# Optimization experiments

Measured on AMD Instinct MI355X. Metric: run time of the kernel, lower is better.

## Reference

```python
import jax, jax.numpy as jnp
import numpy as np

WS = 7        # window size (cubic)
SHIFT = 3     # shift size (cubic)
NH = 6        # num heads
EPS = 1e-5


def _layernorm(x, g, b):
    m = x.mean(-1, keepdims=True)
    v = ((x - m) ** 2).mean(-1, keepdims=True)
    return (x - m) / jnp.sqrt(v + EPS) * g + b


def _win_partition(x, ws):
    # (B,H,W,T,C) -> (B*nW, ws^3, C)
    B, H, W, T, C = x.shape
    x = x.reshape(B, H // ws, ws, W // ws, ws, T // ws, ws, C)
    return x.transpose(0, 1, 3, 5, 2, 4, 6, 7).reshape(-1, ws * ws * ws, C)


def _win_reverse(w, ws, B, H, W, T):
    # (B*nW, ws^3, C) -> (B,H,W,T,C)
    C = w.shape[-1]
    x = w.reshape(B, H // ws, W // ws, T // ws, ws, ws, ws, C)
    return x.transpose(0, 1, 4, 2, 5, 3, 6, 7).reshape(B, H, W, T, C)


def _rel_index(ws):
    # 3D relative position index, (N, N) int, N = ws^3 (torch.meshgrid default 'ij')
    coords = np.stack(np.meshgrid(np.arange(ws), np.arange(ws), np.arange(ws), indexing='ij'))
    cf = coords.reshape(3, -1)
    rel = (cf[:, :, None] - cf[:, None, :]).transpose(1, 2, 0)
    rel[:, :, 0] += ws - 1
    rel[:, :, 1] += ws - 1
    rel[:, :, 2] += ws - 1
    rel[:, :, 0] *= (2 * ws - 1) ** 2
    rel[:, :, 1] *= (2 * ws - 1)
    return rel.sum(-1)


def _compute_mask(Hp, Wp, Tp, ws, shift):
    img = np.zeros((1, Hp, Wp, Tp, 1), np.float32)
    cnt = 0
    sl = (slice(0, -ws), slice(-ws, -shift), slice(-shift, None))
    for h in sl:
        for w in sl:
            for t in sl:
                img[:, h, w, t, :] = cnt
                cnt += 1
    mw = np.asarray(_win_partition(jnp.asarray(img), ws)).reshape(-1, ws ** 3)  # (nW, N)
    am = mw[:, None, :] - mw[:, :, None]
    return jnp.asarray(np.where(am != 0, -100.0, 0.0).astype(np.float32))


def setup_inputs() -> dict:
    key = jax.random.key(0)
    ks = jax.random.split(key, 10)
    B, Hd, Wd, Td, C = 2, 28, 28, 28, 192
    L = Hd * Wd * Td
    Ch = int(C * 4.0)
    s = 0.02
    inp = {
        'x': jax.random.normal(ks[0], (B, L, C), jnp.float32),
        'mask': _compute_mask(Hd, Wd, Td, WS, SHIFT),
        'gamma1': jnp.ones((C,), jnp.float32),
        'beta1': jnp.zeros((C,), jnp.float32),
        'qkv_w': jax.random.normal(ks[1], (3 * C, C), jnp.float32) * s,
        'qkv_b': jnp.zeros((3 * C,), jnp.float32),
        'rpb_table': jax.random.normal(ks[2], ((2 * WS - 1) ** 3, NH), jnp.float32) * s,
        'proj_w': jax.random.normal(ks[3], (C, C), jnp.float32) * s,
        'proj_b': jnp.zeros((C,), jnp.float32),
        'gamma2': jnp.ones((C,), jnp.float32),
        'beta2': jnp.zeros((C,), jnp.float32),
        'fc1_w': jax.random.normal(ks[4], (Ch, C), jnp.float32) * s,
        'fc1_b': jnp.zeros((Ch,), jnp.float32),
        'fc2_w': jax.random.normal(ks[5], (C, Ch), jnp.float32) * s,
        'fc2_b': jnp.zeros((C,), jnp.float32),
        'H': Hd, 'W': Wd, 'T': Td,
    }
    return inp


def reference(x, mask, gamma1, beta1, qkv_w, qkv_b, rpb_table, proj_w, proj_b,
              gamma2, beta2, fc1_w, fc1_b, fc2_w, fc2_b, H, W, T):
    B, L, C = x.shape
    hd = C // NH
    scale = hd ** -0.5
    shortcut = x

    h1 = _layernorm(x, gamma1, beta1).reshape(B, H, W, T, C)
    # H,W,T are multiples of WS -> no padding; cyclic shift for SW-MSA
    shifted = jnp.roll(h1, (-SHIFT, -SHIFT, -SHIFT), axis=(1, 2, 3))
    xw = _win_partition(shifted, WS)            # (B*nW, N, C)
    Bn, N, _ = xw.shape

    qkv = (xw @ qkv_w.T + qkv_b).reshape(Bn, N, 3, NH, hd).transpose(2, 0, 3, 1, 4)
    q, k, v = qkv[0] * scale, qkv[1], qkv[2]     # (Bn, NH, N, hd)
    attn = jnp.einsum('bhnd,bhmd->bhnm', q, k)   # (Bn, NH, N, N)

    idx = _rel_index(WS)
    bias = rpb_table[idx.reshape(-1)].reshape(N, N, NH).transpose(2, 0, 1)
    attn = attn + bias[None]

    nW = mask.shape[0]
    attn = attn.reshape(Bn // nW, nW, NH, N, N) + mask[None, :, None]
    attn = jax.nn.softmax(attn.reshape(Bn, NH, N, N), axis=-1)

    out = jnp.einsum('bhnm,bhmd->bhnd', attn, v).transpose(0, 2, 1, 3).reshape(Bn, N, C)
    out = out @ proj_w.T + proj_b

    shifted = _win_reverse(out, WS, B, H, W, T)
    xr = jnp.roll(shifted, (SHIFT, SHIFT, SHIFT), axis=(1, 2, 3)).reshape(B, L, C)

    x = shortcut + xr
    h2 = _layernorm(x, gamma2, beta2)
    m = jax.nn.gelu(h2 @ fc1_w.T + fc1_b, approximate=False)
    return x + (m @ fc2_w.T + fc2_b)
```

## Files before the change

### kernel.cpp

```cpp
#include <hip/hip_runtime.h>
#include <hip/hip_bf16.h>

typedef unsigned short u16;
typedef unsigned int u32;
typedef __attribute__((ext_vector_type(8))) short s16x8;
typedef __attribute__((ext_vector_type(4))) float f32x4;

__device__ __forceinline__ float bf2f(u16 v) {
    union { u32 u; float f; } x; x.u = ((u32)v) << 16; return x.f;
}
__device__ __forceinline__ u16 f2bf(float f) {
    union { float f; u32 u; } x; x.f = f;
    u32 r = x.u + 0x7fffu + ((x.u >> 16) & 1u);
    return (u16)(r >> 16);
}
__device__ __forceinline__ u32 f2bf_pk(float a, float b) {
    return (u32)f2bf(a) | ((u32)f2bf(b) << 16);
}
__device__ __forceinline__ void gl2lds(const u16* g, u16* l) {
    __builtin_amdgcn_global_load_lds(
        (const __attribute__((address_space(1))) unsigned int*)g,
        (__attribute__((address_space(3))) unsigned int*)l, 16, 0, 0);
}

#define L_TOK 21952
#define C_DIM 192
#define LOG2E 1.4426950408889634f
#define Q2SCALE 0.2550565444463649f
#define BT_STR 352

__global__ __launch_bounds__(256) void cvt_k(const float* __restrict__ s0,
                                             const float* __restrict__ s1,
                                             const float* __restrict__ s2,
                                             const float* __restrict__ s3,
                                             u16* __restrict__ dst)
{
    int i = blockIdx.x * 256 + threadIdx.x;
    float v;
    if (i < 110592) v = s0[i];
    else if (i < 147456) v = s1[i - 110592];
    else if (i < 294912) v = s2[i - 147456];
    else v = s3[i - 294912];
    dst[i] = f2bf(v);
}

__global__ __launch_bounds__(256) void bias6_k(const float* __restrict__ rpb,
                                               u16* __restrict__ bias6T)
{
    const int n = blockIdx.x * 256 + threadIdx.x;
    if (n >= BT_STR) return;
    const int m = blockIdx.y, hh = blockIdx.z;
    u16 v = 0;
    if (n <= 342) {
        int hq = n / 49, r1 = n - hq * 49, wq = r1 / 7, tq = r1 - wq * 7;
        int hm = m / 49, r2 = m - hm * 49, wm = r2 / 7, tm = r2 - wm * 7;
        int idx = ((hq - hm + 6) * 13 + (wq - wm + 6)) * 13 + (tq - tm + 6);
        v = f2bf(rpb[idx * 6 + hh] * LOG2E);
    }
    bias6T[((size_t)hh * 343 + m) * BT_STR + n] = v;
}

template<int MODE>
__global__ __launch_bounds__(256) void ln_k(const float* __restrict__ in,
                                            const float* __restrict__ g,
                                            const float* __restrict__ b,
                                            u16* __restrict__ out)
{
    const int lane = threadIdx.x & 63, wv = threadIdx.x >> 6;
    const int tok = blockIdx.x * 4 + wv;
    size_t base = (size_t)tok * C_DIM;
    float x0 = in[base + lane];
    float x1 = in[base + 64 + lane];
    float x2 = in[base + 128 + lane];
    float s = x0 + x1 + x2;
    float sq = x0 * x0 + x1 * x1 + x2 * x2;
    #pragma unroll
    for (int off = 32; off > 0; off >>= 1) {
        s += __shfl_xor(s, off, 64);
        sq += __shfl_xor(sq, off, 64);
    }
    const float mean = s * (1.0f / 192.0f);
    float var = sq * (1.0f / 192.0f) - mean * mean;
    var = fmaxf(var, 0.0f);
    const float rstd = rsqrtf(var + 1e-5f);

    size_t obase;
    if (MODE == 0) {
        int bi = tok / L_TOK;
        int l = tok - bi * L_TOK;
        int h = l / 784;
        int rm = l - h * 784;
        int w = rm / 28;
        int t = rm - w * 28;
        int hs = h + 25; if (hs >= 28) hs -= 28;
        int ws = w + 25; if (ws >= 28) ws -= 28;
        int ts = t + 25; if (ts >= 28) ts -= 28;
        int win = ((bi * 4 + hs / 7) * 4 + ws / 7) * 4 + ts / 7;
        int n = (hs % 7) * 49 + (ws % 7) * 7 + (ts % 7);
        obase = ((size_t)win * 343 + n) * C_DIM;
    } else {
        obase = base;
    }
    #pragma unroll
    for (int i = 0; i < 3; i++) {
        int c = lane + i * 64;
        float xv = (i == 0) ? x0 : (i == 1) ? x1 : x2;
        float y = (xv - mean) * rstd * g[c] + b[c];
        out[obase + c] = f2bf(y);
    }
}

template<int K, int EPI>
__global__ __launch_bounds__(256) void gemm_k(const u16* __restrict__ A,
                                              const u16* __restrict__ W,
                                              const float* __restrict__ bias,
                                              void* __restrict__ outp,
                                              const void* __restrict__ resp,
                                              int Ncols)
{
    __shared__ __align__(16) u16 As[3 * 128 * 32];
    __shared__ __align__(16) u16 Bs[3 * 64 * 32];
    const int t = threadIdx.x;
    const int bm = blockIdx.y;
    const int n0 = blockIdx.x * 64;
    const int lane = t & 63, wv = t >> 6;
    const int wm = (wv >> 1) * 64, wn = (wv & 1) * 32;
    const int r16 = lane & 15, quad = lane >> 4;

    f32x4 acc[4][2];
    #pragma unroll
    for (int i = 0; i < 4; i++)
        #pragma unroll
        for (int j = 0; j < 2; j++) acc[i][j] = (f32x4){0.f, 0.f, 0.f, 0.f};

    const int ar = t >> 2, ac = (t & 3) * 8;
    const size_t abase = (size_t)bm * 128 * K;

    for (int kc = 0; kc < K; kc += 96) {
        if (kc) __syncthreads();
        #pragma unroll
        for (int kt = 0; kt < 3; kt++) {
            const int k0 = kc + kt * 32;
            gl2lds(&A[abase + (size_t)ar * K + k0 + ac], &As[kt * 4096 + 8 * t]);
            gl2lds(&A[abase + (size_t)(ar + 64) * K + k0 + ac], &As[kt * 4096 + 2048 + 8 * t]);
            gl2lds(&W[(size_t)(n0 + ar) * K + k0 + ac], &Bs[kt * 2048 + 8 * t]);
        }
        __syncthreads();
        #pragma unroll
        for (int kt = 0; kt < 3; kt++) {
            s16x8 af[4], bf[2];
            #pragma unroll
            for (int fm = 0; fm < 4; fm++)
                af[fm] = *(const s16x8*)&As[kt * 4096 + (wm + fm * 16 + r16) * 32 + quad * 8];
            #pragma unroll
            for (int fn = 0; fn < 2; fn++)
                bf[fn] = *(const s16x8*)&Bs[kt * 2048 + (wn + fn * 16 + r16) * 32 + quad * 8];
            #pragma unroll
            for (int fm = 0; fm < 4; fm++)
                #pragma unroll
                for (int fn = 0; fn < 2; fn++)
                    acc[fm][fn] = __builtin_amdgcn_mfma_f32_16x16x32_bf16(af[fm], bf[fn], acc[fm][fn], 0, 0, 0);
        }
    }

    #pragma unroll
    for (int fm = 0; fm < 4; fm++) {
        #pragma unroll
        for (int fn = 0; fn < 2; fn++) {
            #pragma unroll
            for (int r = 0; r < 4; r++) {
                const int grow = bm * 128 + wm + fm * 16 + quad * 4 + r;
                const int gcol = n0 + wn + fn * 16 + r16;
                float v = acc[fm][fn][r] + bias[gcol];
                if (EPI == 0) {
                    if (gcol < 192) v *= Q2SCALE;
                    ((u16*)outp)[(size_t)grow * Ncols + gcol] = f2bf(v);
                } else if (EPI == 1) {
                    v = 0.5f * v * (1.0f + erff(v * 0.70710678118654752f));
                    ((u16*)outp)[(size_t)grow * Ncols + gcol] = f2bf(v);
                } else if (EPI == 2) {
                    size_t o = (size_t)grow * C_DIM + gcol;
                    ((float*)outp)[o] = v + ((const float*)resp)[o];
                } else {
                    int win = grow / 343, n = grow - win * 343;
                    int bi = win >> 6, wi = win & 63;
                    int hw = wi >> 4, ww = (wi >> 2) & 3, tw = wi & 3;
                    int ph = n / 49, rem = n - ph * 49;
                    int pw = rem / 7, pt = rem - pw * 7;
                    int h = hw * 7 + ph + 3; if (h >= 28) h -= 28;
                    int w = ww * 7 + pw + 3; if (w >= 28) w -= 28;
                    int tt = tw * 7 + pt + 3; if (tt >= 28) tt -= 28;
                    int l = (h * 28 + w) * 28 + tt;
                    size_t o = ((size_t)bi * L_TOK + l) * C_DIM + gcol;
                    ((float*)outp)[o] = v + ((const float*)resp)[o];
                }
            }
        }
    }
}

__global__ __launch_bounds__(256, 2) void attn_k(const u16* __restrict__ qkv,
                                                 const u16* __restrict__ bias6T,
                                                 u16* __restrict__ out)
{
    __shared__ __align__(16) u16 Ks[352 * 40];
    __shared__ __align__(16) u16 Vt[32 * 360];
    __shared__ __align__(16) u16 Pb[4][16 * 40];
    __shared__ u16 Cn[344];

    const int hh = blockIdx.x;
    const int win = blockIdx.y;
    const int wi = win & 63;
    const int t = threadIdx.x, lane = t & 63, wv = t >> 6;
    const int r16 = lane & 15, quad = lane >> 4;
    const size_t qbase = (size_t)win * 343 * 576 + hh * 32;

    for (int j = t; j < 343 * 4; j += 256) {
        int m = j >> 2, ch = j & 3;
        *(uint4*)&Ks[m * 40 + ch * 8] = *(const uint4*)&qkv[qbase + (size_t)m * 576 + 192 + ch * 8];
    }
    if (t < 36) {
        int m = 343 + (t >> 2), ch = t & 3;
        *(uint4*)&Ks[m * 40 + ch * 8] = (uint4){0u, 0u, 0u, 0u};
    }
    for (int i = t; i < 343 * 16; i += 256) {
        int m = i >> 4, d2 = (i & 15) * 2;
        int pm = (m & ~31) + 2 * (m & 15) + ((m >> 4) & 1);
        u32 w2 = *(const u32*)&qkv[qbase + (size_t)m * 576 + 384 + d2];
        Vt[d2 * 360 + pm] = (u16)(w2 & 0xffffu);
        Vt[(d2 + 1) * 360 + pm] = (u16)(w2 >> 16);
    }
    for (int i = t; i < 32 * 9; i += 256) {
        int d = i / 9, m = 343 + i % 9;
        int pm = (m & ~31) + 2 * (m & 15) + ((m >> 4) & 1);
        Vt[d * 360 + pm] = 0;
    }
    {
        const int hw = (wi >> 4) & 3, ww = (wi >> 2) & 3, tw = wi & 3;
        for (int n = t; n < 344; n += 256) {
            int nn = n > 342 ? 342 : n;
            int ph = nn / 49, rem = nn - ph * 49;
            int pw = rem / 7, pt = rem - pw * 7;
            int rh = (hw == 3) ? (ph < 4 ? 1 : 2) : 0;
            int rw = (ww == 3) ? (pw < 4 ? 1 : 2) : 0;
            int rt = (tw == 3) ? (pt < 4 ? 1 : 2) : 0;
            Cn[n] = (u16)(rh * 9 + rw * 3 + rt);
        }
    }
    __syncthreads();

    const u16* biashT = bias6T + (size_t)hh * 343 * BT_STR;

    u16 cntc[22];
    #pragma unroll
    for (int fn = 0; fn < 22; fn++) {
        int col = fn * 16 + r16; if (col > 342) col = 342;
        cntc[fn] = Cn[col];
    }

    for (int qt = 0; qt < 6; qt++) {
        const int row0 = qt * 64 + wv * 16;
        if (row0 > 342) continue;
        int qrow = row0 + r16; if (qrow > 342) qrow = 342;
        s16x8 qa = *(const s16x8*)&qkv[qbase + (size_t)qrow * 576 + quad * 8];

        const int n0 = row0 + quad * 4;
        u16 cr[4];
        #pragma unroll
        for (int r = 0; r < 4; r++) {
            int n = n0 + r; if (n > 342) n = 342;
            cr[r] = Cn[n];
        }

        f32x4 sacc[22];
        #pragma unroll
        for (int fn = 0; fn < 22; fn++) {
            int col = fn * 16 + r16; if (col > 342) col = 342;
            uint2 bv = *(const uint2*)&biashT[(size_t)col * BT_STR + n0];
            sacc[fn][0] = bf2f((u16)(bv.x & 0xffffu));
            sacc[fn][1] = bf2f((u16)(bv.x >> 16));
            sacc[fn][2] = bf2f((u16)(bv.y & 0xffffu));
            sacc[fn][3] = bf2f((u16)(bv.y >> 16));
        }
        #pragma unroll
        for (int fn = 0; fn < 22; fn++) {
            s16x8 kb = *(const s16x8*)&Ks[(fn * 16 + r16) * 40 + quad * 8];
            sacc[fn] = __builtin_amdgcn_mfma_f32_16x16x32_bf16(qa, kb, sacc[fn], 0, 0, 0);
        }

        float rowsum[4] = {0.f, 0.f, 0.f, 0.f};
        #pragma unroll
        for (int fn = 0; fn < 22; fn++) {
            const int col = fn * 16 + r16;
            #pragma unroll
            for (int r = 0; r < 4; r++) {
                float p = 0.0f;
                if (col < 343 && cntc[fn] == cr[r])
                    p = exp2f(fminf(sacc[fn][r], 42.0f));
                sacc[fn][r] = p;
                rowsum[r] += p;
            }
        }
        #pragma unroll
        for (int r = 0; r < 4; r++) {
            float v = rowsum[r];
            #pragma unroll
            for (int off = 1; off < 16; off <<= 1) v += __shfl_xor(v, off, 64);
            rowsum[r] = v;
        }

        u16* pw = &Pb[wv][0];
        u32* pw32 = (u32*)pw;
        f32x4 oacc0 = (f32x4){0.f, 0.f, 0.f, 0.f};
        f32x4 oacc1 = (f32x4){0.f, 0.f, 0.f, 0.f};
        #pragma unroll
        for (int c = 0; c < 11; c++) {
            asm volatile("s_waitcnt lgkmcnt(0)" ::: "memory");
            #pragma unroll
            for (int r = 0; r < 4; r++)
                pw32[(quad * 4 + r) * 20 + r16] = f2bf_pk(sacc[2 * c][r], sacc[2 * c + 1][r]);
            asm volatile("s_waitcnt lgkmcnt(0)" ::: "memory");
            s16x8 pa = *(const s16x8*)&pw[r16 * 40 + quad * 8];
            s16x8 vb0 = *(const s16x8*)&Vt[r16 * 360 + c * 32 + quad * 8];
            s16x8 vb1 = *(const s16x8*)&Vt[(16 + r16) * 360 + c * 32 + quad * 8];
            oacc0 = __builtin_amdgcn_mfma_f32_16x16x32_bf16(pa, vb0, oacc0, 0, 0, 0);
            oacc1 = __builtin_amdgcn_mfma_f32_16x16x32_bf16(pa, vb1, oacc1, 0, 0, 0);
        }

        #pragma unroll
        for (int r = 0; r < 4; r++) {
            const int n = n0 + r;
            if (n < 343) {
                const float rs = rowsum[r];
                const float inv = rs > 0.0f ? 1.0f / rs : 0.0f;
                size_t o = ((size_t)win * 343 + n) * C_DIM + hh * 32;
                out[o + r16] = f2bf(oacc0[r] * inv);
                out[o + 16 + r16] = f2bf(oacc1[r] * inv);
            }
        }
    }
}

extern "C" void kernel_launch(void* const* d_in, const int* in_sizes, int n_in,
                              void* d_out, int out_size, void* d_ws, size_t ws_size,
                              hipStream_t stream)
{
    const float* x      = (const float*)d_in[0];
    const float* g1     = (const float*)d_in[2];
    const float* b1     = (const float*)d_in[3];
    const float* qkv_w  = (const float*)d_in[4];
    const float* qkv_b  = (const float*)d_in[5];
    const float* rpb    = (const float*)d_in[6];
    const float* proj_w = (const float*)d_in[7];
    const float* proj_b = (const float*)d_in[8];
    const float* g2     = (const float*)d_in[9];
    const float* b2     = (const float*)d_in[10];
    const float* fc1_w  = (const float*)d_in[11];
    const float* fc1_b  = (const float*)d_in[12];
    const float* fc2_w  = (const float*)d_in[13];
    const float* fc2_b  = (const float*)d_in[14];

    char* ws = (char*)d_ws;
    u16* xw        = (u16*)(ws + 0);
    u16* bias6T    = (u16*)(ws + 0);
    u16* qkv       = (u16*)(ws + 16861184);
    u16* a1        = (u16*)(ws + 0);
    u16* attn_out  = (u16*)(ws + 67444736);
    u16* h2        = attn_out;
    float* x2      = (float*)(ws + 84305920);
    u16* wbf       = (u16*)(ws + 118028288);
    u16* qkv_wb = wbf;
    u16* proj_wb = wbf + 110592;
    u16* fc1_wb = wbf + 147456;
    u16* fc2_wb = wbf + 294912;

    cvt_k<<<dim3(1728), 256, 0, stream>>>(qkv_w, proj_w, fc1_w, fc2_w, wbf);
    ln_k<0><<<dim3(10976), 256, 0, stream>>>(x, g1, b1, xw);
    gemm_k<192, 0><<<dim3(9, 343), 256, 0, stream>>>(xw, qkv_wb, qkv_b, qkv, nullptr, 576);
    bias6_k<<<dim3(2, 343, 6), 256, 0, stream>>>(rpb, bias6T);
    attn_k<<<dim3(6, 128), 256, 0, stream>>>(qkv, bias6T, attn_out);
    gemm_k<192, 3><<<dim3(3, 343), 256, 0, stream>>>(attn_out, proj_wb, proj_b, x2, x, 192);
    ln_k<1><<<dim3(10976), 256, 0, stream>>>(x2, g2, b2, h2);
    gemm_k<192, 1><<<dim3(12, 343), 256, 0, stream>>>(h2, fc1_wb, fc1_b, a1, nullptr, 768);
    gemm_k<768, 2><<<dim3(3, 343), 256, 0, stream>>>(a1, fc2_wb, fc2_b, d_out, x2, 192);
}
```

Before: 367.1 us.

## Fold shift mask into precomputed per-window-type bias tables

Precomputes 48 bias tables (6 heads × 8 window boundary types) that combine the relative position bias, the shifted-window mask and padding. This removes the per-element mask compare and column bound checks from the attention softmax loop, along with the Cn shared array. It also shrinks the K tile stride from 40 to 32 and raises launch bounds to 3 blocks per CU. In exchange the bias tables take more memory and a larger prep kernel, the stride-32 K reads may hit LDS bank conflicts, and masked entries now go through exp2 rather than being zeroed explicitly.

After: 360.4 us. Within noise of the previous version (-1.8%).

```diff
diff --git a/kernel.cpp b/kernel.cpp
--- a/kernel.cpp
+++ b/kernel.cpp
@@ -15,7 +15,11 @@
     return (u16)(r >> 16);
 }
 __device__ __forceinline__ u32 f2bf_pk(float a, float b) {
-    return (u32)f2bf(a) | ((u32)f2bf(b) << 16);
+    u32 ua = __builtin_bit_cast(u32, a);
+    u32 ub = __builtin_bit_cast(u32, b);
+    ua += 0x7fffu + ((ua >> 16) & 1u);
+    ub += 0x7fffu + ((ub >> 16) & 1u);
+    return __builtin_amdgcn_perm(ub, ua, 0x07060302);
 }
 __device__ __forceinline__ void gl2lds(const u16* g, u16* l) {
     __builtin_amdgcn_global_load_lds(
@@ -44,20 +48,32 @@
     dst[i] = f2bf(v);
 }
 
-__global__ __launch_bounds__(256) void bias6_k(const float* __restrict__ rpb,
-                                               u16* __restrict__ bias6T)
+__global__ __launch_bounds__(256) void bias48_k(const float* __restrict__ rpb,
+                                                u16* __restrict__ biasT)
 {
     const int n = blockIdx.x * 256 + threadIdx.x;
     if (n >= BT_STR) return;
-    const int m = blockIdx.y, hh = blockIdx.z;
-    u16 v = 0;
-    if (n <= 342) {
+    const int m = blockIdx.y;
+    const int z = blockIdx.z;
+    const int hh = z >> 3, wt = z & 7;
+    u16 v;
+    if (n <= 342 && m <= 342) {
         int hq = n / 49, r1 = n - hq * 49, wq = r1 / 7, tq = r1 - wq * 7;
         int hm = m / 49, r2 = m - hm * 49, wm = r2 / 7, tm = r2 - wm * 7;
         int idx = ((hq - hm + 6) * 13 + (wq - wm + 6)) * 13 + (tq - tm + 6);
-        v = f2bf(rpb[idx * 6 + hh] * LOG2E);
-    }
-    bias6T[((size_t)hh * 343 + m) * BT_STR + n] = v;
+        float b = rpb[idx * 6 + hh];
+        int rq = ((wt & 4) ? (hq < 4 ? 1 : 2) : 0) * 9
+               + ((wt & 2) ? (wq < 4 ? 1 : 2) : 0) * 3
+               + ((wt & 1) ? (tq < 4 ? 1 : 2) : 0);
+        int rm = ((wt & 4) ? (hm < 4 ? 1 : 2) : 0) * 9
+               + ((wt & 2) ? (wm < 4 ? 1 : 2) : 0) * 3
+               + ((wt & 1) ? (tm < 4 ? 1 : 2) : 0);
+        if (rq != rm) b -= 100.0f;
+        v = f2bf(b * LOG2E);
+    } else {
+        v = f2bf(-100000.0f);
+    }
+    biasT[((size_t)z * 352 + m) * BT_STR + n] = v;
 }
 
 template<int MODE>
@@ -199,14 +215,13 @@
     }
 }
 
-__global__ __launch_bounds__(256, 2) void attn_k(const u16* __restrict__ qkv,
-                                                 const u16* __restrict__ bias6T,
+__global__ __launch_bounds__(256, 3) void attn_k(const u16* __restrict__ qkv,
+                                                 const u16* __restrict__ biasAll,
                                                  u16* __restrict__ out)
 {
-    __shared__ __align__(16) u16 Ks[352 * 40];
+    __shared__ __align__(16) u16 Ks[352 * 32];
     __shared__ __align__(16) u16 Vt[32 * 360];
     __shared__ __align__(16) u16 Pb[4][16 * 40];
-    __shared__ u16 Cn[344];
 
     const int hh = blockIdx.x;
     const int win = blockIdx.y;
@@ -217,11 +232,11 @@
 
     for (int j = t; j < 343 * 4; j += 256) {
         int m = j >> 2, ch = j & 3;
-        *(uint4*)&Ks[m * 40 + ch * 8] = *(const uint4*)&qkv[qbase + (size_t)m * 576 + 192 + ch * 8];
+        *(uint4*)&Ks[m * 32 + ch * 8] = *(const uint4*)&qkv[qbase + (size_t)m * 576 + 192 + ch * 8];
     }
     if (t < 36) {
         int m = 343 + (t >> 2), ch = t & 3;
-        *(uint4*)&Ks[m * 40 + ch * 8] = (uint4){0u, 0u, 0u, 0u};
+        *(uint4*)&Ks[m * 32 + ch * 8] = (uint4){0u, 0u, 0u, 0u};
     }
     for (int i = t; i < 343 * 16; i += 256) {
         int m = i >> 4, d2 = (i & 15) * 2;
@@ -235,28 +250,11 @@
         int pm = (m & ~31) + 2 * (m & 15) + ((m >> 4) & 1);
         Vt[d * 360 + pm] = 0;
     }
-    {
-        const int hw = (wi >> 4) & 3, ww = (wi >> 2) & 3, tw = wi & 3;
-        for (int n = t; n < 344; n += 256) {
-            int nn = n > 342 ? 342 : n;
-            int ph = nn / 49, rem = nn - ph * 49;
-            int pw = rem / 7, pt = rem - pw * 7;
-            int rh = (hw == 3) ? (ph < 4 ? 1 : 2) : 0;
-            int rw = (ww == 3) ? (pw < 4 ? 1 : 2) : 0;
-            int rt = (tw == 3) ? (pt < 4 ? 1 : 2) : 0;
-            Cn[n] = (u16)(rh * 9 + rw * 3 + rt);
-        }
-    }
     __syncthreads();
 
-    const u16* biashT = bias6T + (size_t)hh * 343 * BT_STR;
-
-    u16 cntc[22];
-    #pragma unroll
-    for (int fn = 0; fn < 22; fn++) {
-        int col = fn * 16 + r16; if (col > 342) col = 342;
-        cntc[fn] = Cn[col];
-    }
+    const int wt = (((wi >> 4) == 3) ? 4 : 0) | ((((wi >> 2) & 3) == 3) ? 2 : 0)
+                 | (((wi & 3) == 3) ? 1 : 0);
+    const u16* biashT = biasAll + (size_t)(hh * 8 + wt) * 352 * BT_STR;
 
     for (int qt = 0; qt < 6; qt++) {
         const int row0 = qt * 64 + wv * 16;
@@ -265,17 +263,11 @@
         s16x8 qa = *(const s16x8*)&qkv[qbase + (size_t)qrow * 576 + quad * 8];
 
         const int n0 = row0 + quad * 4;
-        u16 cr[4];
-        #pragma unroll
-        for (int r = 0; r < 4; r++) {
-            int n = n0 + r; if (n > 342) n = 342;
-            cr[r] = Cn[n];
-        }
 
         f32x4 sacc[22];
         #pragma unroll
         for (int fn = 0; fn < 22; fn++) {
-            int col = fn * 16 + r16; if (col > 342) col = 342;
+            const int col = fn * 16 + r16;
             uint2 bv = *(const uint2*)&biashT[(size_t)col * BT_STR + n0];
             sacc[fn][0] = bf2f((u16)(bv.x & 0xffffu));
             sacc[fn][1] = bf2f((u16)(bv.x >> 16));
@@ -284,19 +276,16 @@
         }
         #pragma unroll
         for (int fn = 0; fn < 22; fn++) {
-            s16x8 kb = *(const s16x8*)&Ks[(fn * 16 + r16) * 40 + quad * 8];
+            s16x8 kb = *(const s16x8*)&Ks[(fn * 16 + r16) * 32 + quad * 8];
             sacc[fn] = __builtin_amdgcn_mfma_f32_16x16x32_bf16(qa, kb, sacc[fn], 0, 0, 0);
         }
 
         float rowsum[4] = {0.f, 0.f, 0.f, 0.f};
         #pragma unroll
         for (int fn = 0; fn < 22; fn++) {
-            const int col = fn * 16 + r16;
             #pragma unroll
             for (int r = 0; r < 4; r++) {
-                float p = 0.0f;
-                if (col < 343 && cntc[fn] == cr[r])
-                    p = exp2f(fminf(sacc[fn][r], 42.0f));
+                float p = exp2f(fminf(sacc[fn][r], 42.0f));
                 sacc[fn][r] = p;
                 rowsum[r] += p;
             }
@@ -362,7 +351,7 @@
 
     char* ws = (char*)d_ws;
     u16* xw        = (u16*)(ws + 0);
-    u16* bias6T    = (u16*)(ws + 0);
+    u16* biasT     = (u16*)(ws + 0);
     u16* qkv       = (u16*)(ws + 16861184);
     u16* a1        = (u16*)(ws + 0);
     u16* attn_out  = (u16*)(ws + 67444736);
@@ -377,8 +366,8 @@
     cvt_k<<<dim3(1728), 256, 0, stream>>>(qkv_w, proj_w, fc1_w, fc2_w, wbf);
     ln_k<0><<<dim3(10976), 256, 0, stream>>>(x, g1, b1, xw);
     gemm_k<192, 0><<<dim3(9, 343), 256, 0, stream>>>(xw, qkv_wb, qkv_b, qkv, nullptr, 576);
-    bias6_k<<<dim3(2, 343, 6), 256, 0, stream>>>(rpb, bias6T);
-    attn_k<<<dim3(6, 128), 256, 0, stream>>>(qkv, bias6T, attn_out);
+    bias48_k<<<dim3(2, 352, 48), 256, 0, stream>>>(rpb, biasT);
+    attn_k<<<dim3(6, 128), 256, 0, stream>>>(qkv, biasT, attn_out);
     gemm_k<192, 3><<<dim3(3, 343), 256, 0, stream>>>(attn_out, proj_wb, proj_b, x2, x, 192);
     ln_k<1><<<dim3(10976), 256, 0, stream>>>(x2, g2, b2, h2);
     gemm_k<192, 1><<<dim3(12, 343), 256, 0, stream>>>(h2, fc1_wb, fc1_b, a1, nullptr, 768);
```
